# Optimization experiments

Measured on AMD Instinct MI355X. Metric: run time of the kernel, lower is better.

The kernel has to match this reference:

```python
import jax, jax.numpy as jnp
import numpy as np

PATCH = 14
DIM = 512
LEVELS = 6
ITERS = LEVELS * 2  # default iters
TOKEN_ATTEND_SELF_VALUE = -0.0005


def setup_inputs() -> dict:
    key = jax.random.key(0)
    ks = jax.random.split(key, 9)
    b = 8
    # weights scaled down (~1/sqrt(dim)) so 12 iterations stay finite in fp32
    s = 0.02
    return {
        "img": jax.random.normal(ks[0], (b, 3, 224, 224), jnp.float32),
        "W_patch": jax.random.normal(ks[1], (PATCH * PATCH * 3, DIM), jnp.float32) * s,
        "b_patch": jax.random.normal(ks[2], (DIM,), jnp.float32) * s,
        "pos_emb": jax.random.normal(ks[3], (256, DIM), jnp.float32) * s,
        "init_levels": jax.random.normal(ks[4], (LEVELS, DIM), jnp.float32),
        "bu_in": jax.random.normal(ks[5], (LEVELS - 1, DIM, 4 * DIM), jnp.float32) * s,
        "bu_out": jax.random.normal(ks[6], (LEVELS - 1, 4 * DIM, DIM), jnp.float32) * s,
        "td_in": jax.random.normal(ks[7], (LEVELS - 1, DIM, 4 * DIM), jnp.float32) * s,
        "td_out": jax.random.normal(ks[8], (LEVELS - 1, 4 * DIM, DIM), jnp.float32) * s,
    }


def _grouped_ff(x, w_in, w_out):
    # x: [b, n, groups, d]; per-group two-layer FF with exact GELU
    h = jnp.einsum('bnld,lde->bnle', x, w_in)
    h = jax.nn.gelu(h, approximate=False)
    return jnp.einsum('bnld,lde->bnle', h, w_out)


def _consensus(levels):
    # levels: [b, n, l, d]; attend_self=False, no local radius
    n, d = levels.shape[1], levels.shape[-1]
    norm = jnp.maximum(jnp.linalg.norm(levels, axis=-1, keepdims=True), 1e-12)
    k = levels / norm
    sim = jnp.einsum('bild,bjld->blij', levels, k) * (d ** -0.5)
    eye = jnp.eye(n, dtype=bool)[None, None]
    sim = jnp.where(eye, jnp.asarray(TOKEN_ATTEND_SELF_VALUE, sim.dtype), sim)
    attn = jax.nn.softmax(sim, axis=-1)
    return jnp.einsum('blij,bjld->bild', attn, levels)


def reference(img, W_patch, b_patch, pos_emb, init_levels, bu_in, bu_out, td_in, td_out):
    b, c, H, W = img.shape
    p = PATCH
    h, w = H // p, W // p
    # 'b c (h p1) (w p2) -> b (h w) (p1 p2 c)'
    x = img.reshape(b, c, h, p, w, p).transpose(0, 2, 4, 3, 5, 1).reshape(b, h * w, p * p * c)
    tokens = x @ W_patch + b_patch  # [b, n, d]
    n = tokens.shape[1]
    pos = pos_emb[:n][None, :, None, :]       # [1, n, 1, d]
    bottom = tokens[:, :, None, :]            # [b, n, 1, d]
    levels = jnp.broadcast_to(init_levels[None, None], (b, n, LEVELS, DIM))

    for _ in range(ITERS):
        lwi = jnp.concatenate([bottom, levels], axis=2)            # [b, n, L+1, d]
        bu = _grouped_ff(lwi[:, :, 1:-1], bu_in, bu_out)           # [b, n, L-1, d]
        td = _grouped_ff(lwi[:, :, 2:] + pos, td_in, td_out)       # [b, n, L-1, d]
        bu = jnp.concatenate([bottom, bu], axis=2)                 # [b, n, L, d]
        td = jnp.pad(td, ((0, 0), (0, 0), (0, 1), (0, 0)))         # [b, n, L, d]
        cons = _consensus(levels)
        levels = (levels + bu + td + cons) * 0.25
    return levels
```

## Files before the change

### kernel.cpp

```cpp
#include <hip/hip_runtime.h>
#include <hip/hip_bf16.h>
#include <math.h>

#define B_   8
#define N_   256
#define L_   6
#define D_   512
#define NT_  2048
#define HID_ 2048

typedef __attribute__((ext_vector_type(4))) float f32x4;
typedef __attribute__((ext_vector_type(8))) short bf16x8;

struct bf16x4s { __hip_bfloat16 x, y, z, w; };

__device__ __forceinline__ bf16x4s to_bf4(float a, float b, float c, float d) {
    bf16x4s r;
    r.x = __float2bfloat16(a); r.y = __float2bfloat16(b);
    r.z = __float2bfloat16(c); r.w = __float2bfloat16(d);
    return r;
}

__device__ __forceinline__ void gload16(const void* g, void* l) {
    __builtin_amdgcn_global_load_lds(
        (const __attribute__((address_space(1))) int*)g,
        (__attribute__((address_space(3))) int*)l, 16, 0, 0);
}

template<int BM, int BN, int WM, int WN, typename CT, bool GELU, bool ACCUM>
__global__ __launch_bounds__(512, 4) void gemm_ff(
    const __hip_bfloat16* __restrict__ A, int lda, long az,
    const __hip_bfloat16* __restrict__ B, int ldb, long bz,
    CT* __restrict__ C, int ldc, long cz, int K)
{
    constexpr int WVM = BM / WM, WVN = BN / WN;
    constexpr int MR = WVM / 16, NR = WVN / 16;
    constexpr int ALOADS = (BM * 64) / (512 * 8);
    constexpr int BLOADS = (BN * 64) / (512 * 8);
    constexpr int LOADS  = ALOADS + BLOADS;

    __shared__ short As[2][BM * 64];
    __shared__ short Bs[2][BN * 64];

    const int tid = threadIdx.x;
    const int wv = tid >> 6, lane = tid & 63;
    const int wr = wv / WN, wc = wv % WN;

    const int gx = gridDim.x, gy = gridDim.y;
    const int nwg = gx * gy * gridDim.z;
    int lid = (blockIdx.z * gy + blockIdx.y) * gx + blockIdx.x;
    lid = (lid & 7) * (nwg >> 3) + (lid >> 3);
    const int bx = lid % gx, by = (lid / gx) % gy, bzz = lid / (gx * gy);

    A += (long)bzz * az;  B += (long)bzz * bz;  C += (long)bzz * cz;
    const int m0 = by * BM, n0 = bx * BN;

    f32x4 acc[MR][NR] = {};

    const int srow_a = tid >> 3, sslot = tid & 7;

#define STAGE(BUF, K0)                                                        \
    {                                                                         \
        _Pragma("unroll")                                                     \
        for (int i = 0; i < ALOADS; ++i) {                                    \
            const int row = srow_a + i * 64;                                  \
            const int gs  = sslot ^ (row & 7);                                \
            gload16(A + (long)(m0 + row) * lda + (K0) + gs * 8,               \
                    &As[BUF][(wv * 64 + i * 512) * 8]);                       \
        }                                                                     \
        _Pragma("unroll")                                                     \
        for (int i = 0; i < BLOADS; ++i) {                                    \
            const int row = srow_a + i * 64;                                  \
            const int gs  = sslot ^ (row & 7);                                \
            gload16(B + (long)(n0 + row) * ldb + (K0) + gs * 8,               \
                    &Bs[BUF][(wv * 64 + i * 512) * 8]);                       \
        }                                                                     \
    }

    const int fr = lane & 15, k4 = lane >> 4;
    const int nt = K / 64;
    int cur = 0;

    STAGE(0, 0);

    for (int t = 0; t < nt; ++t) {
        if (t + 1 < nt) {
            STAGE(cur ^ 1, (t + 1) * 64);
            asm volatile("s_waitcnt vmcnt(%0)\n\ts_barrier"
                         :: "n"(LOADS) : "memory");
        } else {
            asm volatile("s_waitcnt vmcnt(0)\n\ts_barrier" ::: "memory");
        }

#pragma unroll
        for (int ks = 0; ks < 2; ++ks) {
            bf16x8 af[MR], bf[NR];
#pragma unroll
            for (int i = 0; i < MR; ++i) {
                const int r = wr * WVM + i * 16 + fr;
                af[i] = *(const bf16x8*)&As[cur][r * 64 + ((ks * 4 + k4) ^ (r & 7)) * 8];
            }
#pragma unroll
            for (int j = 0; j < NR; ++j) {
                const int r = wc * WVN + j * 16 + fr;
                bf[j] = *(const bf16x8*)&Bs[cur][r * 64 + ((ks * 4 + k4) ^ (r & 7)) * 8];
            }
            __builtin_amdgcn_s_setprio(1);
#pragma unroll
            for (int i = 0; i < MR; ++i)
#pragma unroll
                for (int j = 0; j < NR; ++j)
                    acc[i][j] = __builtin_amdgcn_mfma_f32_16x16x32_bf16(
                        af[i], bf[j], acc[i][j], 0, 0, 0);
            __builtin_amdgcn_s_setprio(0);
        }
        asm volatile("s_waitcnt lgkmcnt(0)\n\ts_barrier" ::: "memory");
        cur ^= 1;
    }
#undef STAGE

    const int cr4 = (lane >> 4) * 4, cc = lane & 15;
#pragma unroll
    for (int i = 0; i < MR; ++i)
#pragma unroll
        for (int j = 0; j < NR; ++j) {
            const int col = n0 + wc * WVN + j * 16 + cc;
#pragma unroll
            for (int r = 0; r < 4; ++r) {
                const int row = m0 + wr * WVM + i * 16 + cr4 + r;
                float v = acc[i][j][r];
                if (GELU) v = 0.5f * v * (1.0f + erff(v * 0.70710678118654752f));
                CT* p = &C[(long)row * ldc + col];
                if constexpr (ACCUM) *p = *p + (CT)v;
                else if constexpr (sizeof(CT) == 2) *p = __float2bfloat16(v);
                else *p = (CT)v;
            }
        }
}

__device__ __forceinline__ void mfma_kloop(
    const __hip_bfloat16* __restrict__ A, int lda,
    const __hip_bfloat16* __restrict__ B, int ldb,
    int m0, int n0, int K, short* As, short* Bs,
    f32x4 acc[4][4], int wave, int lane)
{
    const int srow_in = lane >> 2;
    const int sslot   = lane & 3;
    const int wm = (wave >> 1) * 64, wn = (wave & 1) * 64;

    for (int k0 = 0; k0 < K; k0 += 32) {
        __syncthreads();
#pragma unroll
        for (int c = 0; c < 2; ++c) {
            const int rbase = c * 64 + wave * 16;
            const int row   = rbase + srow_in;
            const int gk    = sslot ^ ((row >> 1) & 3);
            gload16(A + (long)(m0 + row) * lda + k0 + gk * 8, As + rbase * 32);
            gload16(B + (long)(n0 + row) * ldb + k0 + gk * 8, Bs + rbase * 32);
        }
        __syncthreads();

        const int fr = lane & 15, ksub = lane >> 4;
        bf16x8 af[4], bfr[4];
#pragma unroll
        for (int i = 0; i < 4; ++i) {
            const int ra = wm + i * 16 + fr;
            af[i]  = *(const bf16x8*)(As + ra * 32 + (ksub ^ ((ra >> 1) & 3)) * 8);
            const int rb = wn + i * 16 + fr;
            bfr[i] = *(const bf16x8*)(Bs + rb * 32 + (ksub ^ ((rb >> 1) & 3)) * 8);
        }
#pragma unroll
        for (int i = 0; i < 4; ++i)
#pragma unroll
            for (int j = 0; j < 4; ++j)
                acc[i][j] = __builtin_amdgcn_mfma_f32_16x16x32_bf16(
                    af[i], bfr[j], acc[i][j], 0, 0, 0);
    }
}

template<typename CT, bool GELU, bool ACCUM>
__global__ __launch_bounds__(256) void gemm_mfma(
    const __hip_bfloat16* __restrict__ A, int lda, long az,
    const __hip_bfloat16* __restrict__ B, int ldb, long bz,
    CT* __restrict__ C, int ldc, long cz, int K,
    const float* __restrict__ bias)
{
    __shared__ short As[128 * 32];
    __shared__ short Bs[128 * 32];
    const int tid = threadIdx.x;
    const int wave = tid >> 6, lane = tid & 63;
    const int z = blockIdx.z;
    A += (long)z * az;  B += (long)z * bz;  C += (long)z * cz;
    const int m0 = blockIdx.y * 128, n0 = blockIdx.x * 128;
    const int wm = (wave >> 1) * 64, wn = (wave & 1) * 64;

    f32x4 acc[4][4] = {};
    mfma_kloop(A, lda, B, ldb, m0, n0, K, As, Bs, acc, wave, lane);

    const int cr = lane >> 4, cc = lane & 15;
#pragma unroll
    for (int j = 0; j < 4; ++j) {
        const int col = n0 + wn + j * 16 + cc;
        const float bv = bias ? bias[col] : 0.f;
#pragma unroll
        for (int i = 0; i < 4; ++i)
#pragma unroll
            for (int r = 0; r < 4; ++r) {
                const int row = m0 + wm + i * 16 + cr * 4 + r;
                float v = acc[i][j][r] + bv;
                if (GELU) v = 0.5f * v * (1.0f + erff(v * 0.70710678118654752f));
                CT* p = &C[(long)row * ldc + col];
                if constexpr (ACCUM) *p = *p + (CT)v;
                else if constexpr (sizeof(CT) == 2) *p = __float2bfloat16(v);
                else *p = (CT)v;
            }
    }
}

__global__ __launch_bounds__(256) void sim_mfma(
    const __hip_bfloat16* __restrict__ lev_bf, const float* __restrict__ invn,
    float* __restrict__ sim)
{
    __shared__ short As[128 * 32];
    __shared__ short Bs[128 * 32];
    const int tid = threadIdx.x;
    const int wave = tid >> 6, lane = tid & 63;
    const int z = blockIdx.z;
    const int b = z / 6, l = z - 6 * b;
    const __hip_bfloat16* base = lev_bf + (long)b * (N_ * L_ * D_) + (long)l * D_;
    const int m0 = blockIdx.y * 128, n0 = blockIdx.x * 128;
    const int wm = (wave >> 1) * 64, wn = (wave & 1) * 64;

    f32x4 acc[4][4] = {};
    mfma_kloop(base, L_ * D_, base, L_ * D_, m0, n0, D_, As, Bs, acc, wave, lane);

    const int cr = lane >> 4, cc = lane & 15;
    const float sc = 0.044194173824159216f;
#pragma unroll
    for (int j = 0; j < 4; ++j) {
        const int jg = n0 + wn + j * 16 + cc;
        const float iv = invn[((long)b * N_ + jg) * L_ + l] * sc;
#pragma unroll
        for (int i = 0; i < 4; ++i)
#pragma unroll
            for (int r = 0; r < 4; ++r) {
                const int ig = m0 + wm + i * 16 + cr * 4 + r;
                float v = acc[i][j][r] * iv;
                if (ig == jg) v = -0.0005f;
                sim[((long)z * N_ + ig) * N_ + jg] = v;
            }
    }
}

__global__ __launch_bounds__(256) void cons_mfma(
    const __hip_bfloat16* __restrict__ attn, const __hip_bfloat16* __restrict__ levT,
    float* __restrict__ cons)
{
    __shared__ short As[128 * 32];
    __shared__ short Bs[128 * 32];
    const int tid = threadIdx.x;
    const int wave = tid >> 6, lane = tid & 63;
    const int z = blockIdx.z;
    const int b = z / 6, l = z - 6 * b;
    const __hip_bfloat16* A = attn + (long)z * N_ * N_;
    const __hip_bfloat16* B = levT + (long)z * D_ * N_;
    float* C = cons + (long)b * (N_ * L_ * D_) + (long)l * D_;
    const int m0 = blockIdx.y * 128, n0 = blockIdx.x * 128;
    const int wm = (wave >> 1) * 64, wn = (wave & 1) * 64;

    f32x4 acc[4][4] = {};
    mfma_kloop(A, N_, B, N_, m0, n0, N_, As, Bs, acc, wave, lane);

    const int cr = lane >> 4, cc = lane & 15;
#pragma unroll
    for (int j = 0; j < 4; ++j) {
        const int col = n0 + wn + j * 16 + cc;
#pragma unroll
        for (int i = 0; i < 4; ++i)
#pragma unroll
            for (int r = 0; r < 4; ++r) {
                const int row = m0 + wm + i * 16 + cr * 4 + r;
                C[(long)row * (L_ * D_) + col] = acc[i][j][r];
            }
    }
}

__global__ __launch_bounds__(256) void transpose_to_bf16(
    const float* __restrict__ src, __hip_bfloat16* __restrict__ dst,
    int R, int Cc)
{
    __shared__ float t[32][33];
    const int zz = blockIdx.z;
    src += (long)zz * R * Cc;  dst += (long)zz * R * Cc;
    const int tx = threadIdx.x & 31, ty = threadIdx.x >> 5;
    const int c0 = blockIdx.x * 32, r0 = blockIdx.y * 32;
#pragma unroll
    for (int i = 0; i < 4; ++i)
        t[ty + i * 8][tx] = src[(long)(r0 + ty + i * 8) * Cc + c0 + tx];
    __syncthreads();
#pragma unroll
    for (int i = 0; i < 4; ++i)
        dst[(long)(c0 + ty + i * 8) * R + r0 + tx] = __float2bfloat16(t[tx][ty + i * 8]);
}

__global__ __launch_bounds__(256) void levT_kernel(
    const float* __restrict__ levels, __hip_bfloat16* __restrict__ levT)
{
    __shared__ float t[32][33];
    const int z = blockIdx.z;
    const int b = z / 6, l = z - 6 * b;
    const float* base = levels + (long)b * (N_ * L_ * D_) + (long)l * D_;
    const int tx = threadIdx.x & 31, ty = threadIdx.x >> 5;
    const int d0 = blockIdx.x * 32, j0 = blockIdx.y * 32;
#pragma unroll
    for (int i = 0; i < 4; ++i)
        t[ty + i * 8][tx] = base[(long)(j0 + ty + i * 8) * (L_ * D_) + d0 + tx];
    __syncthreads();
#pragma unroll
    for (int i = 0; i < 4; ++i)
        levT[(long)z * D_ * N_ + (long)(d0 + ty + i * 8) * N_ + j0 + tx] =
            __float2bfloat16(t[tx][ty + i * 8]);
}

__global__ __launch_bounds__(256) void invnorm_kernel(
    const float* __restrict__ levels, float* __restrict__ invn)
{
    const int wid = blockIdx.x * 4 + (threadIdx.x >> 6);
    const int lane = threadIdx.x & 63;
    const float* row = levels + (long)wid * 512;
    float s = 0.f;
#pragma unroll
    for (int k = lane * 4; k < 512; k += 256) {
        const float4 v = *(const float4*)&row[k];
        s += v.x * v.x + v.y * v.y + v.z * v.z + v.w * v.w;
    }
#pragma unroll
    for (int o = 1; o < 64; o <<= 1) s += __shfl_xor(s, o);
    if (lane == 0) invn[wid] = 1.0f / fmaxf(sqrtf(s), 1e-12f);
}

__global__ __launch_bounds__(256) void softmax_kernel(
    const float* __restrict__ sim, __hip_bfloat16* __restrict__ attn)
{
    const long row = (long)blockIdx.x * 4 + (threadIdx.x >> 6);
    const int lane = threadIdx.x & 63;
    const float* p = sim + row * 256;
    float4 v = *(const float4*)&p[lane * 4];
    float m = fmaxf(fmaxf(v.x, v.y), fmaxf(v.z, v.w));
#pragma unroll
    for (int o = 1; o < 64; o <<= 1) m = fmaxf(m, __shfl_xor(m, o));
    v.x = expf(v.x - m); v.y = expf(v.y - m);
    v.z = expf(v.z - m); v.w = expf(v.w - m);
    float s = v.x + v.y + v.z + v.w;
#pragma unroll
    for (int o = 1; o < 64; o <<= 1) s += __shfl_xor(s, o);
    const float inv = 1.0f / s;
    *(bf16x4s*)&attn[row * 256 + lane * 4] =
        to_bf4(v.x * inv, v.y * inv, v.z * inv, v.w * inv);
}

__global__ __launch_bounds__(256) void patchify_kernel(
    const float* __restrict__ img, __hip_bfloat16* __restrict__ Xp)
{
    const int t = blockIdx.x;
    const int b = t >> 8, n = t & 255;
    const int hh = n >> 4, ww = n & 15;
    for (int k = threadIdx.x; k < 608; k += 256) {
        float v = 0.f;
        if (k < 588) {
            const int c = k % 3;
            const int pj = (k / 3) % 14;
            const int pi = k / 42;
            v = img[(((long)b * 3 + c) * 224 + (hh * 14 + pi)) * 224 + (ww * 14 + pj)];
        }
        Xp[(long)t * 608 + k] = __float2bfloat16(v);
    }
}

__global__ __launch_bounds__(256) void wpT_kernel(
    const float* __restrict__ Wp, __hip_bfloat16* __restrict__ WpT)
{
    __shared__ float t[32][33];
    const int k0 = blockIdx.x * 32, d0 = blockIdx.y * 32;
    const int tx = threadIdx.x & 31, ty = threadIdx.x >> 5;
#pragma unroll
    for (int i = 0; i < 4; ++i) {
        const int k = k0 + ty + i * 8;
        t[ty + i * 8][tx] = (k < 588) ? Wp[(long)k * 512 + d0 + tx] : 0.f;
    }
    __syncthreads();
#pragma unroll
    for (int i = 0; i < 4; ++i)
        WpT[(long)(d0 + ty + i * 8) * 608 + k0 + tx] = __float2bfloat16(t[tx][ty + i * 8]);
}

__global__ __launch_bounds__(256) void init_levels_kernel(
    float* __restrict__ levels, const float* __restrict__ initlv)
{
    const long f = (long)blockIdx.x * 256 + threadIdx.x;
    const int d4 = f & 127;
    const int l = (int)((f >> 7) % 6);
    *(float4*)&levels[f * 4] = *(const float4*)&initlv[(long)l * 512 + d4 * 4];
}

__global__ __launch_bounds__(256) void lev_lp_init(
    const float* __restrict__ levels, const float* __restrict__ pos,
    __hip_bfloat16* __restrict__ lev_bf, __hip_bfloat16* __restrict__ lp_bf)
{
    const long f = (long)blockIdx.x * 256 + threadIdx.x;
    const int d4 = f & 127;
    const long tl = f >> 7;
    const int l = (int)(tl % 6);
    const long t = tl / 6;
    const float4 v = *(const float4*)&levels[f * 4];
    *(bf16x4s*)&lev_bf[f * 4] = to_bf4(v.x, v.y, v.z, v.w);
    if (l >= 1) {
        const float4 p = *(const float4*)&pos[(long)(t & 255) * 512 + d4 * 4];
        *(bf16x4s*)&lp_bf[((t * 5 + l - 1) * 512) + d4 * 4] =
            to_bf4(v.x + p.x, v.y + p.y, v.z + p.z, v.w + p.w);
    }
}

__global__ __launch_bounds__(256) void zero_l0(float* __restrict__ acc)
{
    const long f = (long)blockIdx.x * 256 + threadIdx.x;
    const long t = f >> 7;
    const int d4 = (int)(f & 127);
    *(float4*)&acc[t * 3072 + d4 * 4] = make_float4(0.f, 0.f, 0.f, 0.f);
}

__global__ __launch_bounds__(256) void update_kernel(
    float* __restrict__ levels, const float* __restrict__ tokens,
    const float* __restrict__ acc, const float* __restrict__ cons,
    const float* __restrict__ pos,
    __hip_bfloat16* __restrict__ lev_bf, __hip_bfloat16* __restrict__ lp_bf,
    float* __restrict__ invn)
{
    const int wid = blockIdx.x * 4 + (threadIdx.x >> 6);
    const int lane = threadIdx.x & 63;
    const int l = wid % 6;
    const long t = wid / 6;
    const long rowoff = (long)wid * 512;

    float ss = 0.f;
#pragma unroll
    for (int half = 0; half < 2; ++half) {
        const int k = lane * 4 + half * 256;
        const long off = rowoff + k;
        float4 lev = *(const float4*)&levels[off];
        const float4 cns = *(const float4*)&cons[off];
        float4 ac  = *(const float4*)&acc[off];
        if (l == 0) {
            const float4 bot = *(const float4*)&tokens[t * 512 + k];
            ac.x += bot.x; ac.y += bot.y; ac.z += bot.z; ac.w += bot.w;
        }
        lev.x = (lev.x + ac.x + cns.x) * 0.25f;
        lev.y = (lev.y + ac.y + cns.y) * 0.25f;
        lev.z = (lev.z + ac.z + cns.z) * 0.25f;
        lev.w = (lev.w + ac.w + cns.w) * 0.25f;
        *(float4*)&levels[off] = lev;
        *(bf16x4s*)&lev_bf[off] = to_bf4(lev.x, lev.y, lev.z, lev.w);
        if (l >= 1) {
            const float4 p = *(const float4*)&pos[(long)(t & 255) * 512 + k];
            *(bf16x4s*)&lp_bf[((t * 5 + l - 1) * 512) + k] =
                to_bf4(lev.x + p.x, lev.y + p.y, lev.z + p.z, lev.w + p.w);
        }
        ss += lev.x * lev.x + lev.y * lev.y + lev.z * lev.z + lev.w * lev.w;
    }
#pragma unroll
    for (int o = 1; o < 64; o <<= 1) ss += __shfl_xor(ss, o);
    if (lane == 0) invn[wid] = 1.0f / fmaxf(sqrtf(ss), 1e-12f);
}

extern "C" void kernel_launch(void* const* d_in, const int* in_sizes, int n_in,
                              void* d_out, int out_size, void* d_ws, size_t ws_size,
                              hipStream_t stream)
{
    const float* img    = (const float*)d_in[0];
    const float* Wp     = (const float*)d_in[1];
    const float* bp     = (const float*)d_in[2];
    const float* pos    = (const float*)d_in[3];
    const float* initlv = (const float*)d_in[4];
    const float* bu_in  = (const float*)d_in[5];
    const float* bu_out = (const float*)d_in[6];
    const float* td_in  = (const float*)d_in[7];
    const float* td_out = (const float*)d_in[8];

    float* levels = (float*)d_out;
    float* ws = (float*)d_ws;
    float* tokens  = ws;
    float* acc     = tokens + 1048576;
    float* overlay = acc + 6291456;
    float* invn    = overlay + 10485760;
    __hip_bfloat16* lev_bf  = (__hip_bfloat16*)(invn + 12288);
    __hip_bfloat16* lp_bf   = lev_bf + 6291456;
    __hip_bfloat16* wtin_bu = lp_bf + 5242880;
    __hip_bfloat16* wtout_bu= wtin_bu + 5242880;
    __hip_bfloat16* wtin_td = wtout_bu + 5242880;
    __hip_bfloat16* wtout_td= wtin_td + 5242880;

    __hip_bfloat16* h = (__hip_bfloat16*)overlay;
    float* sim  = overlay;
    float* cons = overlay + 3145728;
    __hip_bfloat16* levT_bf = lev_bf;
    __hip_bfloat16* attn_bf = lp_bf;
    __hip_bfloat16* Xp  = (__hip_bfloat16*)acc;
    __hip_bfloat16* WpT = Xp + 1245184;

    init_levels_kernel<<<6144, 256, 0, stream>>>(levels, initlv);
    lev_lp_init<<<6144, 256, 0, stream>>>(levels, pos, lev_bf, lp_bf);
    invnorm_kernel<<<3072, 256, 0, stream>>>(levels, invn);
    patchify_kernel<<<NT_, 256, 0, stream>>>(img, Xp);
    wpT_kernel<<<dim3(19, 16), 256, 0, stream>>>(Wp, WpT);
    gemm_mfma<float, false, false><<<dim3(4, 16, 1), 256, 0, stream>>>(
        Xp, 608, 0, WpT, 608, 0, tokens, 512, 0, 608, bp);
    transpose_to_bf16<<<dim3(64, 16, 5), 256, 0, stream>>>(bu_in,  wtin_bu,  512, 2048);
    transpose_to_bf16<<<dim3(16, 64, 5), 256, 0, stream>>>(bu_out, wtout_bu, 2048, 512);
    transpose_to_bf16<<<dim3(64, 16, 5), 256, 0, stream>>>(td_in,  wtin_td,  512, 2048);
    transpose_to_bf16<<<dim3(16, 64, 5), 256, 0, stream>>>(td_out, wtout_td, 2048, 512);

    for (int it = 0; it < 12; ++it) {
        gemm_ff<128, 128, 2, 4, __hip_bfloat16, true, false>
            <<<dim3(16, 16, 5), 512, 0, stream>>>(
            lev_bf, L_ * D_, 512,
            wtin_bu, D_, (long)HID_ * D_,
            h, HID_, (long)NT_ * HID_, D_);
        gemm_ff<128, 128, 2, 4, float, false, false>
            <<<dim3(4, 16, 5), 512, 0, stream>>>(
            h, HID_, (long)NT_ * HID_,
            wtout_bu, HID_, (long)D_ * HID_,
            acc + D_, L_ * D_, D_, HID_);
        zero_l0<<<1024, 256, 0, stream>>>(acc);
        gemm_ff<128, 128, 2, 4, __hip_bfloat16, true, false>
            <<<dim3(16, 16, 5), 512, 0, stream>>>(
            lp_bf, 5 * D_, 512,
            wtin_td, D_, (long)HID_ * D_,
            h, HID_, (long)NT_ * HID_, D_);
        gemm_ff<128, 128, 2, 4, float, false, true>
            <<<dim3(4, 16, 5), 512, 0, stream>>>(
            h, HID_, (long)NT_ * HID_,
            wtout_td, HID_, (long)D_ * HID_,
            acc, L_ * D_, D_, HID_);

        sim_mfma<<<dim3(2, 2, 48), 256, 0, stream>>>(lev_bf, invn, sim);
        softmax_kernel<<<3072, 256, 0, stream>>>(sim, attn_bf);
        levT_kernel<<<dim3(16, 8, 48), 256, 0, stream>>>(levels, levT_bf);
        cons_mfma<<<dim3(4, 2, 48), 256, 0, stream>>>(attn_bf, levT_bf, cons);
        update_kernel<<<3072, 256, 0, stream>>>(levels, tokens, acc, cons, pos,
                                                lev_bf, lp_bf, invn);
    }
}
```

Measured before the change: 2.588 ms.

## Merge bottom-up and top-down FF GEMMs into single batched launches

```diff
diff --git a/kernel.cpp b/kernel.cpp
--- a/kernel.cpp
+++ b/kernel.cpp
@@ -27,9 +27,10 @@
         (__attribute__((address_space(3))) int*)l, 16, 0, 0);
 }
 
-template<int BM, int BN, int WM, int WN, typename CT, bool GELU, bool ACCUM>
+template<int BM, int BN, int WM, int WN, typename CT, bool GELU>
 __global__ __launch_bounds__(512, 4) void gemm_ff(
-    const __hip_bfloat16* __restrict__ A, int lda, long az,
+    const __hip_bfloat16* __restrict__ A1, int lda1, long az1,
+    const __hip_bfloat16* __restrict__ A2, int lda2, long az2, int zsplit,
     const __hip_bfloat16* __restrict__ B, int ldb, long bz,
     CT* __restrict__ C, int ldc, long cz, int K)
 {
@@ -52,7 +53,11 @@
     lid = (lid & 7) * (nwg >> 3) + (lid >> 3);
     const int bx = lid % gx, by = (lid / gx) % gy, bzz = lid / (gx * gy);
 
-    A += (long)bzz * az;  B += (long)bzz * bz;  C += (long)bzz * cz;
+    const __hip_bfloat16* A;
+    int lda;
+    if (bzz < zsplit) { A = A1 + (long)bzz * az1;            lda = lda1; }
+    else              { A = A2 + (long)(bzz - zsplit) * az2; lda = lda2; }
+    B += (long)bzz * bz;  C += (long)bzz * cz;
     const int m0 = by * BM, n0 = bx * BN;
 
     f32x4 acc[MR][NR] = {};
@@ -131,8 +136,7 @@
                 float v = acc[i][j][r];
                 if (GELU) v = 0.5f * v * (1.0f + erff(v * 0.70710678118654752f));
                 CT* p = &C[(long)row * ldc + col];
-                if constexpr (ACCUM) *p = *p + (CT)v;
-                else if constexpr (sizeof(CT) == 2) *p = __float2bfloat16(v);
+                if constexpr (sizeof(CT) == 2) *p = __float2bfloat16(v);
                 else *p = (CT)v;
             }
         }
@@ -178,7 +182,7 @@
     }
 }
 
-template<typename CT, bool GELU, bool ACCUM>
+template<typename CT, bool GELU>
 __global__ __launch_bounds__(256) void gemm_mfma(
     const __hip_bfloat16* __restrict__ A, int lda, long az,
     const __hip_bfloat16* __restrict__ B, int ldb, long bz,
@@ -210,8 +214,7 @@
                 float v = acc[i][j][r] + bv;
                 if (GELU) v = 0.5f * v * (1.0f + erff(v * 0.70710678118654752f));
                 CT* p = &C[(long)row * ldc + col];
-                if constexpr (ACCUM) *p = *p + (CT)v;
-                else if constexpr (sizeof(CT) == 2) *p = __float2bfloat16(v);
+                if constexpr (sizeof(CT) == 2) *p = __float2bfloat16(v);
                 else *p = (CT)v;
             }
     }
@@ -421,18 +424,10 @@
     }
 }
 
-__global__ __launch_bounds__(256) void zero_l0(float* __restrict__ acc)
-{
-    const long f = (long)blockIdx.x * 256 + threadIdx.x;
-    const long t = f >> 7;
-    const int d4 = (int)(f & 127);
-    *(float4*)&acc[t * 3072 + d4 * 4] = make_float4(0.f, 0.f, 0.f, 0.f);
-}
-
 __global__ __launch_bounds__(256) void update_kernel(
     float* __restrict__ levels, const float* __restrict__ tokens,
-    const float* __restrict__ acc, const float* __restrict__ cons,
-    const float* __restrict__ pos,
+    const float* __restrict__ acc_bu, const float* __restrict__ acc_td,
+    const float* __restrict__ cons, const float* __restrict__ pos,
     __hip_bfloat16* __restrict__ lev_bf, __hip_bfloat16* __restrict__ lp_bf,
     float* __restrict__ invn)
 {
@@ -449,10 +444,12 @@
         const long off = rowoff + k;
         float4 lev = *(const float4*)&levels[off];
         const float4 cns = *(const float4*)&cons[off];
-        float4 ac  = *(const float4*)&acc[off];
-        if (l == 0) {
-            const float4 bot = *(const float4*)&tokens[t * 512 + k];
-            ac.x += bot.x; ac.y += bot.y; ac.z += bot.z; ac.w += bot.w;
+        float4 ac;
+        if (l == 0) ac = *(const float4*)&tokens[t * 512 + k];
+        else        ac = *(const float4*)&acc_bu[((long)(l - 1) * NT_ + t) * 512 + k];
+        if (l < 5) {
+            const float4 td = *(const float4*)&acc_td[((long)l * NT_ + t) * 512 + k];
+            ac.x += td.x; ac.y += td.y; ac.z += td.z; ac.w += td.w;
         }
         lev.x = (lev.x + ac.x + cns.x) * 0.25f;
         lev.y = (lev.y + ac.y + cns.y) * 0.25f;
@@ -489,22 +486,20 @@
     float* levels = (float*)d_out;
     float* ws = (float*)d_ws;
     float* tokens  = ws;
-    float* acc     = tokens + 1048576;
-    float* overlay = acc + 6291456;
-    float* invn    = overlay + 10485760;
-    __hip_bfloat16* lev_bf  = (__hip_bfloat16*)(invn + 12288);
-    __hip_bfloat16* lp_bf   = lev_bf + 6291456;
-    __hip_bfloat16* wtin_bu = lp_bf + 5242880;
-    __hip_bfloat16* wtout_bu= wtin_bu + 5242880;
-    __hip_bfloat16* wtin_td = wtout_bu + 5242880;
-    __hip_bfloat16* wtout_td= wtin_td + 5242880;
-
-    __hip_bfloat16* h = (__hip_bfloat16*)overlay;
-    float* sim  = overlay;
-    float* cons = overlay + 3145728;
+    float* acc_bu  = tokens + 1048576;
+    float* acc_td  = acc_bu + 5242880;
+    __hip_bfloat16* h = (__hip_bfloat16*)(acc_td + 5242880);
+    float* invn    = (float*)(h + 41943040);
+    __hip_bfloat16* lev_bf   = (__hip_bfloat16*)(invn + 12288);
+    __hip_bfloat16* lp_bf    = lev_bf + 6291456;
+    __hip_bfloat16* wtin_all = lp_bf + 5242880;
+    __hip_bfloat16* wtout_all= wtin_all + 10485760;
+
+    float* sim  = (float*)h;
+    float* cons = sim + 3145728;
     __hip_bfloat16* levT_bf = lev_bf;
     __hip_bfloat16* attn_bf = lp_bf;
-    __hip_bfloat16* Xp  = (__hip_bfloat16*)acc;
+    __hip_bfloat16* Xp  = (__hip_bfloat16*)acc_bu;
     __hip_bfloat16* WpT = Xp + 1245184;
 
     init_levels_kernel<<<6144, 256, 0, stream>>>(levels, initlv);
@@ -512,41 +507,32 @@
     invnorm_kernel<<<3072, 256, 0, stream>>>(levels, invn);
     patchify_kernel<<<NT_, 256, 0, stream>>>(img, Xp);
     wpT_kernel<<<dim3(19, 16), 256, 0, stream>>>(Wp, WpT);
-    gemm_mfma<float, false, false><<<dim3(4, 16, 1), 256, 0, stream>>>(
+    gemm_mfma<float, false><<<dim3(4, 16, 1), 256, 0, stream>>>(
         Xp, 608, 0, WpT, 608, 0, tokens, 512, 0, 608, bp);
-    transpose_to_bf16<<<dim3(64, 16, 5), 256, 0, stream>>>(bu_in,  wtin_bu,  512, 2048);
-    transpose_to_bf16<<<dim3(16, 64, 5), 256, 0, stream>>>(bu_out, wtout_bu, 2048, 512);
-    transpose_to_bf16<<<dim3(64, 16, 5), 256, 0, stream>>>(td_in,  wtin_td,  512, 2048);
-    transpose_to_bf16<<<dim3(16, 64, 5), 256, 0, stream>>>(td_out, wtout_td, 2048, 512);
+    transpose_to_bf16<<<dim3(64, 16, 5), 256, 0, stream>>>(bu_in,  wtin_all, 512, 2048);
+    transpose_to_bf16<<<dim3(64, 16, 5), 256, 0, stream>>>(td_in,  wtin_all + 5242880, 512, 2048);
+    transpose_to_bf16<<<dim3(16, 64, 5), 256, 0, stream>>>(bu_out, wtout_all, 2048, 512);
+    transpose_to_bf16<<<dim3(16, 64, 5), 256, 0, stream>>>(td_out, wtout_all + 5242880, 2048, 512);
 
     for (int it = 0; it < 12; ++it) {
-        gemm_ff<128, 128, 2, 4, __hip_bfloat16, true, false>
-            <<<dim3(16, 16, 5), 512, 0, stream>>>(
+        gemm_ff<128, 128, 2, 4, __hip_bfloat16, true>
+            <<<dim3(16, 16, 10), 512, 0, stream>>>(
             lev_bf, L_ * D_, 512,
-            wtin_bu, D_, (long)HID_ * D_,
+            lp_bf, 5 * D_, 512, 5,
+            wtin_all, D_, (long)HID_ * D_,
             h, HID_, (long)NT_ * HID_, D_);
-        gemm_ff<128, 128, 2, 4, float, false, false>
-            <<<dim3(4, 16, 5), 512, 0, stream>>>(
+        gemm_ff<128, 128, 2, 4, float, false>
+            <<<dim3(4, 16, 10), 512, 0, stream>>>(
             h, HID_, (long)NT_ * HID_,
-            wtout_bu, HID_, (long)D_ * HID_,
-            acc + D_, L_ * D_, D_, HID_);
-        zero_l0<<<1024, 256, 0, stream>>>(acc);
-        gemm_ff<128, 128, 2, 4, __hip_bfloat16, true, false>
-            <<<dim3(16, 16, 5), 512, 0, stream>>>(
-            lp_bf, 5 * D_, 512,
-            wtin_td, D_, (long)HID_ * D_,
-            h, HID_, (long)NT_ * HID_, D_);
-        gemm_ff<128, 128, 2, 4, float, false, true>
-            <<<dim3(4, 16, 5), 512, 0, stream>>>(
-            h, HID_, (long)NT_ * HID_,
-            wtout_td, HID_, (long)D_ * HID_,
-            acc, L_ * D_, D_, HID_);
+            h, HID_, (long)NT_ * HID_, 10,
+            wtout_all, HID_, (long)D_ * HID_,
+            acc_bu, D_, (long)NT_ * D_, HID_);
 
         sim_mfma<<<dim3(2, 2, 48), 256, 0, stream>>>(lev_bf, invn, sim);
         softmax_kernel<<<3072, 256, 0, stream>>>(sim, attn_bf);
         levT_kernel<<<dim3(16, 8, 48), 256, 0, stream>>>(levels, levT_bf);
         cons_mfma<<<dim3(4, 2, 48), 256, 0, stream>>>(attn_bf, levT_bf, cons);
-        update_kernel<<<3072, 256, 0, stream>>>(levels, tokens, acc, cons, pos,
-                                                lev_bf, lp_bf, invn);
-    }
-}
+        update_kernel<<<3072, 256, 0, stream>>>(levels, tokens, acc_bu, acc_td,
+                                                cons, pos, lev_bf, lp_bf, invn);
+    }
+}
```

After: 2.366 ms. -8.6%, faster.
